# Performance work log

Measured on AMD Instinct MI355X. Metric: run time of the kernel, lower is better.

## Reference

```python
import jax, jax.numpy as jnp
import numpy as np

C = 192; G = 12; CG = C // G          # channels, groups, channels per group
KS = 3; PAD = 1; K = KS * KS - 1      # 3x3 kernel, remove_center=True -> 8 points
HID = 4 * C                           # mlp_ratio = 4
OFFSET_SCALE = 1.0

# kernel dilation grid (x, y) pairs, center removed (remove_center=True)
_pts = np.arange(KS) - (KS - 1) // 2
_gx, _gy = np.meshgrid(_pts, _pts, indexing='ij')
_grid = np.stack([_gx.ravel(), _gy.ravel()], -1).astype(np.float32)
_grid = _grid[~np.all(_grid == 0, axis=1)]   # (K, 2)
GRID = jnp.asarray(_grid)


def _ln(x, w, b, eps=1e-5):
    mu = jnp.mean(x, -1, keepdims=True)
    var = jnp.var(x, -1, keepdims=True)
    return (x - mu) * jax.lax.rsqrt(var + eps) * w + b


def _dcnv3(x, in_proj_w, in_proj_b, dw_w, dw_b, dw_ln_w, dw_ln_b,
           off_w, off_b, mask_w, mask_b, cfs_w, cfs_b, out_proj_w, out_proj_b):
    # x: (B, H, W, C) channels-last
    B, H, W, _ = x.shape
    xp = x @ in_proj_w + in_proj_b          # value / x_proj
    # depthwise conv -> LN -> GELU on the raw input (offset/mask branch)
    x1 = jax.lax.conv_general_dilated(
        x, dw_w, (1, 1), 'SAME',
        dimension_numbers=('NHWC', 'HWIO', 'NHWC'),
        feature_group_count=C) + dw_b
    x1 = jax.nn.gelu(_ln(x1, dw_ln_w, dw_ln_b, 1e-6), approximate=False)
    off = (x1 @ off_w + off_b).reshape(B, H, W, G, K, 2)      # (dx, dy) in pixels
    mask = jax.nn.softmax((x1 @ mask_w + mask_b).reshape(B, H, W, G, K), axis=-1)
    # pad value and flatten spatial; (B, Hp*Wp, G, 1, CG)
    Hp, Wp = H + 2 * PAD, W + 2 * PAD
    v = jnp.pad(xp, ((0, 0), (PAD, PAD), (PAD, PAD), (0, 0))).reshape(B, Hp * Wp, G, 1, CG)
    # sampling locations in padded-image pixel index coords (grid_sample align_corners=False)
    bx = jnp.arange(W, dtype=x.dtype)[None, None, :, None, None] + PAD
    by = jnp.arange(H, dtype=x.dtype)[None, :, None, None, None] + PAD
    px = (bx + (GRID[:, 0] + off[..., 0]) * OFFSET_SCALE).reshape(B, H * W, G, K)
    py = (by + (GRID[:, 1] + off[..., 1]) * OFFSET_SCALE).reshape(B, H * W, G, K)
    x0 = jnp.floor(px); y0 = jnp.floor(py)
    wx = px - x0; wy = py - y0
    ix0 = x0.astype(jnp.int32); iy0 = y0.astype(jnp.int32)

    def gather(iy, ix):
        valid = ((iy >= 0) & (iy < Hp) & (ix >= 0) & (ix < Wp)).astype(x.dtype)
        idx = jnp.clip(iy, 0, Hp - 1) * Wp + jnp.clip(ix, 0, Wp - 1)
        s = jnp.take_along_axis(v, idx[..., None], axis=1)    # (B, HW, G, K, CG)
        return s * valid[..., None]

    s = (gather(iy0, ix0)         * ((1 - wy) * (1 - wx))[..., None]
       + gather(iy0, ix0 + 1)     * ((1 - wy) * wx)[..., None]
       + gather(iy0 + 1, ix0)     * (wy * (1 - wx))[..., None]
       + gather(iy0 + 1, ix0 + 1) * (wy * wx)[..., None])
    out = jnp.einsum('bngk,bngkc->bngc', mask.reshape(B, H * W, G, K), s).reshape(B, H, W, C)
    # center feature scale
    cfs = jax.nn.sigmoid(x1 @ cfs_w.T + cfs_b)                # (B, H, W, G)
    cfs = jnp.repeat(cfs, CG, axis=-1)                        # (B, H, W, C)
    out = out * (1 - cfs) + xp * cfs
    return out @ out_proj_w + out_proj_b


def _forward(x, norm1_w, norm1_b, norm2_w, norm2_b, rpn1_w, rpn1_b, rpn2_w, rpn2_b,
             in_proj_w, in_proj_b, dw_w, dw_b, dw_ln_w, dw_ln_b, off_w, off_b,
             mask_w, mask_b, cfs_w, cfs_b, out_proj_w, out_proj_b,
             fc1_w, fc1_b, fc2_w, fc2_b):
    d = _dcnv3(_ln(x, norm1_w, norm1_b), in_proj_w, in_proj_b, dw_w, dw_b,
               dw_ln_w, dw_ln_b, off_w, off_b, mask_w, mask_b, cfs_w, cfs_b,
               out_proj_w, out_proj_b)
    x = x + _ln(d, rpn1_w, rpn1_b)                            # res_post_norm branch 1
    h = jax.nn.gelu(_ln(x, norm2_w, norm2_b) @ fc1_w + fc1_b, approximate=False) @ fc2_w + fc2_b
    x = x + _ln(h, rpn2_w, rpn2_b)                            # res_post_norm branch 2
    return x


def setup_inputs():
    key = jax.random.key(0)
    ks = jax.random.split(key, 12)
    r = lambda i, shape, s=0.02: jax.random.normal(ks[i], shape, jnp.float32) * s
    B, H, W = 4, 56, 56
    return dict(
        x=jax.random.normal(ks[0], (B, H, W, C), jnp.float32),
        norm1_w=jnp.ones((C,)), norm1_b=jnp.zeros((C,)),
        norm2_w=jnp.ones((C,)), norm2_b=jnp.zeros((C,)),
        rpn1_w=jnp.ones((C,)), rpn1_b=jnp.zeros((C,)),
        rpn2_w=jnp.ones((C,)), rpn2_b=jnp.zeros((C,)),
        in_proj_w=r(1, (C, C)), in_proj_b=jnp.zeros((C,)),
        dw_w=r(2, (KS, KS, 1, C), 0.1), dw_b=jnp.zeros((C,)),
        dw_ln_w=jnp.ones((C,)), dw_ln_b=jnp.zeros((C,)),
        off_w=r(3, (C, G * K * 2), 0.1), off_b=jnp.zeros((G * K * 2,)),
        mask_w=r(4, (C, G * K), 0.1), mask_b=jnp.zeros((G * K,)),
        cfs_w=r(5, (G, C), 0.1), cfs_b=jnp.zeros((G,)),
        out_proj_w=r(6, (C, C)), out_proj_b=jnp.zeros((C,)),
        fc1_w=r(7, (C, HID)), fc1_b=jnp.zeros((HID,)),
        fc2_w=r(8, (HID, C)), fc2_b=jnp.zeros((C,)),
    )


def reference(x, norm1_w, norm1_b, norm2_w, norm2_b, rpn1_w, rpn1_b, rpn2_w, rpn2_b,
              in_proj_w, in_proj_b, dw_w, dw_b, dw_ln_w, dw_ln_b, off_w, off_b,
              mask_w, mask_b, cfs_w, cfs_b, out_proj_w, out_proj_b,
              fc1_w, fc1_b, fc2_w, fc2_b):
    return _forward(x, norm1_w, norm1_b, norm2_w, norm2_b, rpn1_w, rpn1_b, rpn2_w, rpn2_b,
                    in_proj_w, in_proj_b, dw_w, dw_b, dw_ln_w, dw_ln_b, off_w, off_b,
                    mask_w, mask_b, cfs_w, cfs_b, out_proj_w, out_proj_b,
                    fc1_w, fc1_b, fc2_w, fc2_b)
```

## Files before the change

kernel.cpp:

```cpp
#include <hip/hip_runtime.h>
#include <hip/hip_bf16.h>
#include <math.h>


#define BATCH 4
#define HH 56
#define WW 56
#define CC 192
#define NPIX (BATCH * HH * WW)
#define XS_STR 200
#define H1S 776
#define OFS 193
#define MLS 97

typedef __hip_bfloat16 bf16;
typedef __attribute__((ext_vector_type(8))) short short8;
typedef __attribute__((ext_vector_type(4))) float float4v;

__device__ __forceinline__ float gelu_exact(float x) {
    return 0.5f * x * (1.f + erff(x * 0.70710678118654752f));
}
__device__ __forceinline__ bf16 f2b(float f) { return __float2bfloat16(f); }
__device__ __forceinline__ float b2fu(short s) {
    return __uint_as_float((unsigned)(unsigned short)s << 16);
}

__global__ __launch_bounds__(256) void prep_w_k(const float* __restrict__ inpw,
        const float* __restrict__ offw, const float* __restrict__ maskw,
        const float* __restrict__ cfsw, const float* __restrict__ outpw,
        const float* __restrict__ fc1w, const float* __restrict__ fc2w,
        bf16* __restrict__ wsB)
{
    const int i = blockIdx.x * 256 + threadIdx.x;
    bf16* inpP = wsB;
    bf16* omP  = wsB + 36864;
    bf16* outP = wsB + 95232;
    bf16* fc1P = wsB + 132096;
    bf16* fc2P = wsB + 279552;
    const int j   = i & 7;
    const int l   = (i >> 3) & 63;
    const int n15 = l & 15, q = l >> 4;
    const int grp = i >> 9;
    if (i < 36864) {
        const int t = grp / 6, c = grp - t * 6;
        const int n = 16 * t + n15, k = 32 * c + 8 * q + j;
        inpP[i] = f2b(inpw[(size_t)k * 192 + n]);
        outP[i] = f2b(outpw[(size_t)k * 192 + n]);
    }
    if (i < 58368) {
        const int t = grp / 6, c = grp - t * 6;
        const int n = 16 * t + n15, k = 32 * c + 8 * q + j;
        omP[i] = (n < 192) ? f2b(offw[(size_t)k * 192 + n])
               : (n < 288) ? f2b(maskw[(size_t)k * 96 + (n - 192)])
               : (n < 300) ? f2b(cfsw[(size_t)(n - 288) * 192 + k])
                           : f2b(0.f);
    }
    if (i < 147456) {
        const int t1 = grp / 6, c1 = grp - t1 * 6;
        const int n1 = 16 * t1 + n15, k1 = 32 * c1 + 8 * q + j;
        fc1P[i] = f2b(fc1w[(size_t)k1 * 768 + n1]);
        const int t2 = grp / 24, c2 = grp - t2 * 24;
        const int n2 = 16 * t2 + n15, k2 = 32 * c2 + 8 * q + j;
        fc2P[i] = f2b(fc2w[(size_t)k2 * 192 + n2]);
    }
}

__global__ __launch_bounds__(256) void ln_gemm8_k(const float* __restrict__ x,
        const float* __restrict__ n1w, const float* __restrict__ n1b,
        const bf16* __restrict__ wP, const float* __restrict__ bias,
        bf16* __restrict__ xn_out, bf16* __restrict__ xp_out)
{
    __shared__ __align__(16) bf16 xs[8 * XS_STR];
    const int tid = threadIdx.x;
    const int w   = tid >> 6;
    const int l   = tid & 63;
    const int n15 = l & 15;
    const int q   = l >> 4;
    const int p0  = blockIdx.x * 8;
    const int c0  = l * 4;

    #pragma unroll
    for (int rr = 0; rr < 2; rr++) {
        const int lr = 2 * w + rr;
        const int base = (p0 + lr) * CC;
        float4 v = (float4){0.f, 0.f, 0.f, 0.f};
        if (l < 48) v = *(const float4*)&x[base + c0];
        float s  = v.x + v.y + v.z + v.w;
        float qq = v.x*v.x + v.y*v.y + v.z*v.z + v.w*v.w;
        #pragma unroll
        for (int off = 32; off > 0; off >>= 1) {
            s  += __shfl_xor(s, off, 64);
            qq += __shfl_xor(qq, off, 64);
        }
        const float mu  = s * (1.f / CC);
        const float var = qq * (1.f / CC) - mu * mu;
        const float rs  = rsqrtf(var + 1e-5f);
        if (l < 48) {
            const float4 nw = *(const float4*)&n1w[c0];
            const float4 nb = *(const float4*)&n1b[c0];
            ushort4 u;
            bf16 h;
            h = f2b((v.x - mu) * rs * nw.x + nb.x); u.x = *(unsigned short*)&h;
            h = f2b((v.y - mu) * rs * nw.y + nb.y); u.y = *(unsigned short*)&h;
            h = f2b((v.z - mu) * rs * nw.z + nb.z); u.z = *(unsigned short*)&h;
            h = f2b((v.w - mu) * rs * nw.w + nb.w); u.w = *(unsigned short*)&h;
            *(ushort4*)&xs[lr * XS_STR + c0] = u;
            *(ushort4*)&xn_out[base + c0] = u;
        }
    }
    __syncthreads();

    short8 aF[6];
    #pragma unroll
    for (int c = 0; c < 6; c++)
        aF[c] = (n15 < 8)
              ? *(const short8*)&xs[n15 * XS_STR + c * 32 + q * 8]
              : (short8){0, 0, 0, 0, 0, 0, 0, 0};

    for (int t = w; t < 12; t += 4) {
        float4v acc = (float4v){0.f, 0.f, 0.f, 0.f};
        #pragma unroll
        for (int c = 0; c < 6; c++) {
            const short8 bF = *(const short8*)&wP[(size_t)((t * 6 + c) * 64 + l) * 8];
            acc = __builtin_amdgcn_mfma_f32_16x16x32_bf16(aF[c], bF, acc, 0, 0, 0);
        }
        if (q < 2) {
            const int n0 = 16 * t;
            const float bb = bias[n0 + n15];
            #pragma unroll
            for (int r = 0; r < 4; r++)
                xp_out[(size_t)(p0 + 4 * q + r) * 192 + n0 + n15] = f2b(acc[r] + bb);
        }
    }
}

__global__ __launch_bounds__(256) void sample_mlp_k(
        const bf16* __restrict__ xp, const bf16* __restrict__ xn,
        const float* __restrict__ dww, const float* __restrict__ dwb,
        const float* __restrict__ dwlnw, const float* __restrict__ dwlnb,
        const bf16* __restrict__ omP, const float* __restrict__ offb,
        const float* __restrict__ maskb, const float* __restrict__ cfsb,
        const bf16* __restrict__ wP, const float* __restrict__ bias,
        const float* __restrict__ x,
        const float* __restrict__ r1w, const float* __restrict__ r1b,
        const float* __restrict__ n2w, const float* __restrict__ n2b,
        const bf16* __restrict__ fc1P, const float* __restrict__ fc1b,
        const bf16* __restrict__ fc2P, const float* __restrict__ fc2b,
        const float* __restrict__ r2w, const float* __restrict__ r2b,
        float* __restrict__ out)
{
    __shared__ __align__(16) bf16 xs[16 * XS_STR];
    __shared__ __align__(16) char uni[16 * H1S * 2];
    __shared__ float ps[4][16], pq[4][16], ps2[4][16], pq2[4][16];

    float (*cv)[192]     = (float(*)[192])uni;
    float (*offs_l)[OFS] = (float(*)[OFS])uni;
    float (*mls_l)[MLS]  = (float(*)[MLS])(uni + 12352);
    float (*cfs_l)[16]   = (float(*)[16])(uni + 18560);
    bf16* h1             = (bf16*)uni;

    const int tid = threadIdx.x;
    const int w   = tid >> 6;
    const int l   = tid & 63;
    const int n15 = l & 15;
    const int q   = l >> 4;
    const int bid = (blockIdx.x & 7) * (NPIX / 128) + (blockIdx.x >> 3);
    const int p0  = bid * 16;

    if (tid < 192) {
        const int px  = tid / 12;
        const int ch0 = (tid - px * 12) * 16;
        const int pix = p0 + px;
        const int bimg = pix / (HH * WW);
        const int hw   = pix - bimg * (HH * WW);
        const int h    = hw / WW;
        const int wx   = hw - h * WW;
        const int ibase = bimg * (HH * WW * CC);

        float a[16];
        #pragma unroll
        for (int j = 0; j < 16; j += 4) {
            const float4 b4 = *(const float4*)&dwb[ch0 + j];
            a[j] = b4.x; a[j+1] = b4.y; a[j+2] = b4.z; a[j+3] = b4.w;
        }
        #pragma unroll
        for (int ky = 0; ky < 3; ky++) {
            const int yy = h + ky - 1;
            if (yy < 0 || yy >= HH) continue;
            #pragma unroll
            for (int kx = 0; kx < 3; kx++) {
                const int xx = wx + kx - 1;
                if (xx < 0 || xx >= WW) continue;
                const int o = ibase + (yy * WW + xx) * CC + ch0;
                const short8 v0 = *(const short8*)&xn[o];
                const short8 v1 = *(const short8*)&xn[o + 8];
                const int wo = (ky * 3 + kx) * CC + ch0;
                const float4 w0 = *(const float4*)&dww[wo];
                const float4 w1 = *(const float4*)&dww[wo + 4];
                const float4 w2 = *(const float4*)&dww[wo + 8];
                const float4 w3 = *(const float4*)&dww[wo + 12];
                a[0]  += b2fu(v0[0]) * w0.x; a[1]  += b2fu(v0[1]) * w0.y;
                a[2]  += b2fu(v0[2]) * w0.z; a[3]  += b2fu(v0[3]) * w0.w;
                a[4]  += b2fu(v0[4]) * w1.x; a[5]  += b2fu(v0[5]) * w1.y;
                a[6]  += b2fu(v0[6]) * w1.z; a[7]  += b2fu(v0[7]) * w1.w;
                a[8]  += b2fu(v1[0]) * w2.x; a[9]  += b2fu(v1[1]) * w2.y;
                a[10] += b2fu(v1[2]) * w2.z; a[11] += b2fu(v1[3]) * w2.w;
                a[12] += b2fu(v1[4]) * w3.x; a[13] += b2fu(v1[5]) * w3.y;
                a[14] += b2fu(v1[6]) * w3.z; a[15] += b2fu(v1[7]) * w3.w;
            }
        }
        #pragma unroll
        for (int j = 0; j < 16; j += 4)
            *(float4*)&cv[px][ch0 + j] = (float4){a[j], a[j+1], a[j+2], a[j+3]};
    }
    __syncthreads();

    #pragma unroll
    for (int pass = 0; pass < 4; pass++) {
        const int px = w + 4 * pass;
        float v[3];
        #pragma unroll
        for (int i = 0; i < 3; i++) v[i] = cv[px][l + 64 * i];
        float s = v[0] + v[1] + v[2];
        float qq = v[0]*v[0] + v[1]*v[1] + v[2]*v[2];
        #pragma unroll
        for (int off = 32; off > 0; off >>= 1) {
            s  += __shfl_xor(s, off, 64);
            qq += __shfl_xor(qq, off, 64);
        }
        const float mu  = s * (1.f / CC);
        const float var = qq * (1.f / CC) - mu * mu;
        const float rs  = rsqrtf(var + 1e-6f);
        #pragma unroll
        for (int i = 0; i < 3; i++) {
            const int c = l + 64 * i;
            xs[px * XS_STR + c] = f2b(gelu_exact((v[i] - mu) * rs * dwlnw[c] + dwlnb[c]));
        }
    }
    __syncthreads();

    {
        short8 aF[6];
        #pragma unroll
        for (int c = 0; c < 6; c++)
            aF[c] = *(const short8*)&xs[n15 * XS_STR + c * 32 + q * 8];

        for (int t = w; t < 19; t += 4) {
            float4v acc = (float4v){0.f, 0.f, 0.f, 0.f};
            #pragma unroll
            for (int c = 0; c < 6; c++) {
                const short8 bF = *(const short8*)&omP[(size_t)((t * 6 + c) * 64 + l) * 8];
                acc = __builtin_amdgcn_mfma_f32_16x16x32_bf16(aF[c], bF, acc, 0, 0, 0);
            }
            if (t < 12) {
                const int n0 = 16 * t;
                const float bb = offb[n0 + n15];
                #pragma unroll
                for (int r = 0; r < 4; r++)
                    offs_l[4 * q + r][n0 + n15] = acc[r] + bb;
            } else if (t < 18) {
                const int m0 = 16 * t - 192;
                const float bb = maskb[m0 + n15];
                #pragma unroll
                for (int r = 0; r < 4; r++) {
                    const float vv = acc[r] + bb;
                    float mx = vv;
                    mx = fmaxf(mx, __shfl_xor(mx, 1, 64));
                    mx = fmaxf(mx, __shfl_xor(mx, 2, 64));
                    mx = fmaxf(mx, __shfl_xor(mx, 4, 64));
                    const float e = __expf(vv - mx);
                    float se = e;
                    se += __shfl_xor(se, 1, 64);
                    se += __shfl_xor(se, 2, 64);
                    se += __shfl_xor(se, 4, 64);
                    mls_l[4 * q + r][m0 + n15] = e * (1.f / se);
                }
            } else {
                const float bb = (n15 < 12) ? cfsb[n15] : 0.f;
                #pragma unroll
                for (int r = 0; r < 4; r++) {
                    const float cf = 1.f / (1.f + __expf(-(acc[r] + bb)));
                    if (n15 < 12) cfs_l[4 * q + r][n15] = cf;
                }
            }
        }
    }
    __syncthreads();

    if (tid < 192) {
        const int px  = tid / 12;
        const int g   = tid - px * 12;
        const int ch0 = g * 16;
        const int pix = p0 + px;
        const int bimg = pix / (HH * WW);
        const int hw   = pix - bimg * (HH * WW);
        const int h    = hw / WW;
        const int wxp  = hw - h * WW;
        const int ibase = bimg * (HH * WW * CC);

        const float cf = cfs_l[px][g];

        float acc[16];
        #pragma unroll
        for (int j = 0; j < 16; j++) acc[j] = 0.f;

        #pragma unroll 2
        for (int k = 0; k < 8; k++) {
            const int kk = k + (k >= 4 ? 1 : 0);
            const int gx = kk / 3 - 1;
            const int gy = kk - (kk / 3) * 3 - 1;
            const float mk  = mls_l[px][g * 8 + k];
            const float px_ = (float)(wxp + gx) + offs_l[px][g * 16 + 2 * k];
            const float py_ = (float)(h   + gy) + offs_l[px][g * 16 + 2 * k + 1];
            const float fx = floorf(px_), fy = floorf(py_);
            const float wxf = px_ - fx, wyf = py_ - fy;
            const int x0 = (int)fx, y0 = (int)fy;
            const float vx0 = ((unsigned)x0       < WW) ? 1.f : 0.f;
            const float vx1 = ((unsigned)(x0 + 1) < WW) ? 1.f : 0.f;
            const float vy0 = ((unsigned)y0       < HH) ? 1.f : 0.f;
            const float vy1 = ((unsigned)(y0 + 1) < HH) ? 1.f : 0.f;
            const int x0c = min(max(x0, 0), WW - 1);
            const int x1c = min(max(x0 + 1, 0), WW - 1);
            const int y0c = min(max(y0, 0), HH - 1);
            const int y1c = min(max(y0 + 1, 0), HH - 1);
            const float wx0 = (1.f - wxf) * vx0, wx1 = wxf * vx1;
            const float wy0 = (1.f - wyf) * vy0, wy1 = wyf * vy1;
            const float w00 = mk * wy0 * wx0, w01 = mk * wy0 * wx1;
            const float w10 = mk * wy1 * wx0, w11 = mk * wy1 * wx1;
            const int r0 = ibase + y0c * (WW * CC) + ch0;
            const int r1 = ibase + y1c * (WW * CC) + ch0;
            const int o00 = r0 + x0c * CC, o01 = r0 + x1c * CC;
            const int o10 = r1 + x0c * CC, o11 = r1 + x1c * CC;
            const short8 a00 = *(const short8*)&xp[o00];
            const short8 b00 = *(const short8*)&xp[o00 + 8];
            const short8 a01 = *(const short8*)&xp[o01];
            const short8 b01 = *(const short8*)&xp[o01 + 8];
            const short8 a10 = *(const short8*)&xp[o10];
            const short8 b10 = *(const short8*)&xp[o10 + 8];
            const short8 a11 = *(const short8*)&xp[o11];
            const short8 b11 = *(const short8*)&xp[o11 + 8];
            #pragma unroll
            for (int j = 0; j < 8; j++) {
                acc[j]     += w00 * b2fu(a00[j]) + w01 * b2fu(a01[j])
                            + w10 * b2fu(a10[j]) + w11 * b2fu(a11[j]);
                acc[8 + j] += w00 * b2fu(b00[j]) + w01 * b2fu(b01[j])
                            + w10 * b2fu(b10[j]) + w11 * b2fu(b11[j]);
            }
        }

        const int po = pix * CC + ch0;
        const short8 xv0 = *(const short8*)&xp[po];
        const short8 xv1 = *(const short8*)&xp[po + 8];
        short8 o0, o1;
        #pragma unroll
        for (int j = 0; j < 8; j++) {
            const float v0 = acc[j]     * (1.f - cf) + b2fu(xv0[j]) * cf;
            const float v1 = acc[8 + j] * (1.f - cf) + b2fu(xv1[j]) * cf;
            bf16 hh;
            hh = f2b(v0); o0[j] = *(short*)&hh;
            hh = f2b(v1); o1[j] = *(short*)&hh;
        }
        *(short8*)&xs[px * XS_STR + ch0]     = o0;
        *(short8*)&xs[px * XS_STR + ch0 + 8] = o1;
    }
    __syncthreads();

    {
        short8 aF[6];
        #pragma unroll
        for (int c = 0; c < 6; c++)
            aF[c] = *(const short8*)&xs[n15 * XS_STR + c * 32 + q * 8];

        float4v acc[3];
        #pragma unroll
        for (int t = 0; t < 3; t++) {
            const int tile = 3 * w + t;
            acc[t] = (float4v){0.f, 0.f, 0.f, 0.f};
            #pragma unroll
            for (int c = 0; c < 6; c++) {
                const short8 bF = *(const short8*)&wP[(size_t)((tile * 6 + c) * 64 + l) * 8];
                acc[t] = __builtin_amdgcn_mfma_f32_16x16x32_bf16(aF[c], bF, acc[t], 0, 0, 0);
            }
            const float bb = bias[16 * tile + n15];
            #pragma unroll
            for (int r = 0; r < 4; r++) acc[t][r] += bb;
        }

        #pragma unroll
        for (int r = 0; r < 4; r++) {
            float sp = acc[0][r] + acc[1][r] + acc[2][r];
            float qp = acc[0][r]*acc[0][r] + acc[1][r]*acc[1][r] + acc[2][r]*acc[2][r];
            #pragma unroll
            for (int o = 1; o < 16; o <<= 1) {
                sp += __shfl_xor(sp, o, 64);
                qp += __shfl_xor(qp, o, 64);
            }
            if (n15 == 0) { ps[w][4 * q + r] = sp; pq[w][4 * q + r] = qp; }
        }
        __syncthreads();

        float x2v[3][4];
        #pragma unroll
        for (int r = 0; r < 4; r++) {
            const int row = 4 * q + r;
            const float s  = ps[0][row] + ps[1][row] + ps[2][row] + ps[3][row];
            const float qq = pq[0][row] + pq[1][row] + pq[2][row] + pq[3][row];
            const float mu  = s * (1.f / CC);
            const float var = qq * (1.f / CC) - mu * mu;
            const float rs  = rsqrtf(var + 1e-5f);
            const size_t grow = p0 + row;
            #pragma unroll
            for (int t = 0; t < 3; t++) {
                const int col = 48 * w + 16 * t + n15;
                x2v[t][r] = x[grow * CC + col] + (acc[t][r] - mu) * rs * r1w[col] + r1b[col];
            }
        }
        #pragma unroll
        for (int r = 0; r < 4; r++) {
            float sp = x2v[0][r] + x2v[1][r] + x2v[2][r];
            float qp = x2v[0][r]*x2v[0][r] + x2v[1][r]*x2v[1][r] + x2v[2][r]*x2v[2][r];
            #pragma unroll
            for (int o = 1; o < 16; o <<= 1) {
                sp += __shfl_xor(sp, o, 64);
                qp += __shfl_xor(qp, o, 64);
            }
            if (n15 == 0) { ps2[w][4 * q + r] = sp; pq2[w][4 * q + r] = qp; }
        }
        __syncthreads();

        #pragma unroll
        for (int r = 0; r < 4; r++) {
            const int row = 4 * q + r;
            const float s  = ps2[0][row] + ps2[1][row] + ps2[2][row] + ps2[3][row];
            const float qq = pq2[0][row] + pq2[1][row] + pq2[2][row] + pq2[3][row];
            const float mu  = s * (1.f / CC);
            const float var = qq * (1.f / CC) - mu * mu;
            const float rs  = rsqrtf(var + 1e-5f);
            #pragma unroll
            for (int t = 0; t < 3; t++) {
                const int col = 48 * w + 16 * t + n15;
                xs[row * XS_STR + col] = f2b((x2v[t][r] - mu) * rs * n2w[col] + n2b[col]);
            }
        }
        __syncthreads();

        short8 aF2[6];
        #pragma unroll
        for (int c = 0; c < 6; c++)
            aF2[c] = *(const short8*)&xs[n15 * XS_STR + c * 32 + q * 8];

        #pragma unroll
        for (int t1 = 0; t1 < 12; t1++) {
            const int tile = 12 * w + t1;
            float4v a1 = (float4v){0.f, 0.f, 0.f, 0.f};
            #pragma unroll
            for (int c = 0; c < 6; c++) {
                const short8 bF = *(const short8*)&fc1P[(size_t)((tile * 6 + c) * 64 + l) * 8];
                a1 = __builtin_amdgcn_mfma_f32_16x16x32_bf16(aF2[c], bF, a1, 0, 0, 0);
            }
            const int n0 = 16 * tile;
            const float bb = fc1b[n0 + n15];
            #pragma unroll
            for (int r = 0; r < 4; r++)
                h1[(4 * q + r) * H1S + n0 + n15] = f2b(gelu_exact(a1[r] + bb));
        }
        __syncthreads();

        float4v acc2[3];
        #pragma unroll
        for (int t = 0; t < 3; t++) acc2[t] = (float4v){0.f, 0.f, 0.f, 0.f};
        #pragma unroll 4
        for (int kc = 0; kc < 24; kc++) {
            const short8 a2 = *(const short8*)&h1[n15 * H1S + kc * 32 + q * 8];
            #pragma unroll
            for (int t = 0; t < 3; t++) {
                const int tile = 3 * w + t;
                const short8 bF = *(const short8*)&fc2P[(size_t)((tile * 24 + kc) * 64 + l) * 8];
                acc2[t] = __builtin_amdgcn_mfma_f32_16x16x32_bf16(a2, bF, acc2[t], 0, 0, 0);
            }
        }
        #pragma unroll
        for (int t = 0; t < 3; t++) {
            const float bb = fc2b[48 * w + 16 * t + n15];
            #pragma unroll
            for (int r = 0; r < 4; r++) acc2[t][r] += bb;
        }

        #pragma unroll
        for (int r = 0; r < 4; r++) {
            float sp = acc2[0][r] + acc2[1][r] + acc2[2][r];
            float qp = acc2[0][r]*acc2[0][r] + acc2[1][r]*acc2[1][r] + acc2[2][r]*acc2[2][r];
            #pragma unroll
            for (int o = 1; o < 16; o <<= 1) {
                sp += __shfl_xor(sp, o, 64);
                qp += __shfl_xor(qp, o, 64);
            }
            if (n15 == 0) { ps[w][4 * q + r] = sp; pq[w][4 * q + r] = qp; }
        }
        __syncthreads();

        #pragma unroll
        for (int r = 0; r < 4; r++) {
            const int row = 4 * q + r;
            const float s  = ps[0][row] + ps[1][row] + ps[2][row] + ps[3][row];
            const float qq = pq[0][row] + pq[1][row] + pq[2][row] + pq[3][row];
            const float mu  = s * (1.f / CC);
            const float var = qq * (1.f / CC) - mu * mu;
            const float rs  = rsqrtf(var + 1e-5f);
            const size_t grow = p0 + row;
            #pragma unroll
            for (int t = 0; t < 3; t++) {
                const int col = 48 * w + 16 * t + n15;
                out[grow * CC + col] = x2v[t][r]
                                     + (acc2[t][r] - mu) * rs * r2w[col] + r2b[col];
            }
        }
    }
}

extern "C" void kernel_launch(void* const* d_in, const int* in_sizes, int n_in,
                              void* d_out, int out_size, void* d_ws, size_t ws_size,
                              hipStream_t stream) {
    const float* x      = (const float*)d_in[0];
    const float* n1w    = (const float*)d_in[1];
    const float* n1b    = (const float*)d_in[2];
    const float* n2w    = (const float*)d_in[3];
    const float* n2b    = (const float*)d_in[4];
    const float* rpn1w  = (const float*)d_in[5];
    const float* rpn1b  = (const float*)d_in[6];
    const float* rpn2w  = (const float*)d_in[7];
    const float* rpn2b  = (const float*)d_in[8];
    const float* inpw   = (const float*)d_in[9];
    const float* inpb   = (const float*)d_in[10];
    const float* dww    = (const float*)d_in[11];
    const float* dwb    = (const float*)d_in[12];
    const float* dwlnw  = (const float*)d_in[13];
    const float* dwlnb  = (const float*)d_in[14];
    const float* offw   = (const float*)d_in[15];
    const float* offb   = (const float*)d_in[16];
    const float* maskw  = (const float*)d_in[17];
    const float* maskb  = (const float*)d_in[18];
    const float* cfsw   = (const float*)d_in[19];
    const float* cfsb   = (const float*)d_in[20];
    const float* outpw  = (const float*)d_in[21];
    const float* outpb  = (const float*)d_in[22];
    const float* fc1w   = (const float*)d_in[23];
    const float* fc1b   = (const float*)d_in[24];
    const float* fc2w   = (const float*)d_in[25];
    const float* fc2b   = (const float*)d_in[26];

    const int N = NPIX;
    const size_t NP = (size_t)N * CC;
    bf16* B0  = (bf16*)d_ws;
    bf16* B1  = B0 + NP;
    bf16* wsB = B1 + NP;
    const bf16* inpP = wsB;
    const bf16* omP  = wsB + 36864;
    const bf16* outP = wsB + 95232;
    const bf16* fc1P = wsB + 132096;
    const bf16* fc2P = wsB + 279552;

    const int g16 = N / 16;

    prep_w_k<<<576, 256, 0, stream>>>(inpw, offw, maskw, cfsw, outpw, fc1w, fc2w, wsB);
    ln_gemm8_k<<<N / 8, 256, 0, stream>>>(x, n1w, n1b, inpP, inpb, B0, B1);
    sample_mlp_k<<<g16, 256, 0, stream>>>(B1, B0, dww, dwb, dwlnw, dwlnb,
                                          omP, offb, maskb, cfsb,
                                          outP, outpb, x, rpn1w, rpn1b,
                                          n2w, n2b, fc1P, fc1b, fc2P, fc2b,
                                          rpn2w, rpn2b, (float*)d_out);
}
```

Measured before the change: 179.9 us.

## Double block size of fused sample/MLP kernel to 512 threads with 8 waves

New measurement: 210.3 us. +16.9%, slower.

```diff
diff --git a/kernel.cpp b/kernel.cpp
--- a/kernel.cpp
+++ b/kernel.cpp
@@ -134,7 +134,7 @@
     }
 }
 
-__global__ __launch_bounds__(256) void sample_mlp_k(
+__global__ __launch_bounds__(512) void sample_mlp_k(
         const bf16* __restrict__ xp, const bf16* __restrict__ xn,
         const float* __restrict__ dww, const float* __restrict__ dwb,
         const float* __restrict__ dwlnw, const float* __restrict__ dwlnb,
@@ -151,7 +151,7 @@
 {
     __shared__ __align__(16) bf16 xs[16 * XS_STR];
     __shared__ __align__(16) char uni[16 * H1S * 2];
-    __shared__ float ps[4][16], pq[4][16], ps2[4][16], pq2[4][16];
+    __shared__ float ps[8][16], pq[8][16], ps2[8][16], pq2[8][16];
 
     float (*cv)[192]     = (float(*)[192])uni;
     float (*offs_l)[OFS] = (float(*)[OFS])uni;
@@ -167,9 +167,10 @@
     const int bid = (blockIdx.x & 7) * (NPIX / 128) + (blockIdx.x >> 3);
     const int p0  = bid * 16;
 
-    if (tid < 192) {
-        const int px  = tid / 12;
-        const int ch0 = (tid - px * 12) * 16;
+    if (tid < 384) {
+        const int px  = tid / 24;
+        const int c8  = tid - px * 24;
+        const int ch0 = c8 * 8;
         const int pix = p0 + px;
         const int bimg = pix / (HH * WW);
         const int hw   = pix - bimg * (HH * WW);
@@ -177,11 +178,12 @@
         const int wx   = hw - h * WW;
         const int ibase = bimg * (HH * WW * CC);
 
-        float a[16];
-        #pragma unroll
-        for (int j = 0; j < 16; j += 4) {
-            const float4 b4 = *(const float4*)&dwb[ch0 + j];
-            a[j] = b4.x; a[j+1] = b4.y; a[j+2] = b4.z; a[j+3] = b4.w;
+        float a[8];
+        {
+            const float4 b0 = *(const float4*)&dwb[ch0];
+            const float4 b1 = *(const float4*)&dwb[ch0 + 4];
+            a[0]=b0.x; a[1]=b0.y; a[2]=b0.z; a[3]=b0.w;
+            a[4]=b1.x; a[5]=b1.y; a[6]=b1.z; a[7]=b1.w;
         }
         #pragma unroll
         for (int ky = 0; ky < 3; ky++) {
@@ -191,33 +193,24 @@
             for (int kx = 0; kx < 3; kx++) {
                 const int xx = wx + kx - 1;
                 if (xx < 0 || xx >= WW) continue;
-                const int o = ibase + (yy * WW + xx) * CC + ch0;
-                const short8 v0 = *(const short8*)&xn[o];
-                const short8 v1 = *(const short8*)&xn[o + 8];
+                const short8 v0 = *(const short8*)&xn[ibase + (yy * WW + xx) * CC + ch0];
                 const int wo = (ky * 3 + kx) * CC + ch0;
                 const float4 w0 = *(const float4*)&dww[wo];
                 const float4 w1 = *(const float4*)&dww[wo + 4];
-                const float4 w2 = *(const float4*)&dww[wo + 8];
-                const float4 w3 = *(const float4*)&dww[wo + 12];
-                a[0]  += b2fu(v0[0]) * w0.x; a[1]  += b2fu(v0[1]) * w0.y;
-                a[2]  += b2fu(v0[2]) * w0.z; a[3]  += b2fu(v0[3]) * w0.w;
-                a[4]  += b2fu(v0[4]) * w1.x; a[5]  += b2fu(v0[5]) * w1.y;
-                a[6]  += b2fu(v0[6]) * w1.z; a[7]  += b2fu(v0[7]) * w1.w;
-                a[8]  += b2fu(v1[0]) * w2.x; a[9]  += b2fu(v1[1]) * w2.y;
-                a[10] += b2fu(v1[2]) * w2.z; a[11] += b2fu(v1[3]) * w2.w;
-                a[12] += b2fu(v1[4]) * w3.x; a[13] += b2fu(v1[5]) * w3.y;
-                a[14] += b2fu(v1[6]) * w3.z; a[15] += b2fu(v1[7]) * w3.w;
-            }
-        }
-        #pragma unroll
-        for (int j = 0; j < 16; j += 4)
-            *(float4*)&cv[px][ch0 + j] = (float4){a[j], a[j+1], a[j+2], a[j+3]};
+                a[0] += b2fu(v0[0]) * w0.x; a[1] += b2fu(v0[1]) * w0.y;
+                a[2] += b2fu(v0[2]) * w0.z; a[3] += b2fu(v0[3]) * w0.w;
+                a[4] += b2fu(v0[4]) * w1.x; a[5] += b2fu(v0[5]) * w1.y;
+                a[6] += b2fu(v0[6]) * w1.z; a[7] += b2fu(v0[7]) * w1.w;
+            }
+        }
+        *(float4*)&cv[px][ch0]     = (float4){a[0], a[1], a[2], a[3]};
+        *(float4*)&cv[px][ch0 + 4] = (float4){a[4], a[5], a[6], a[7]};
     }
     __syncthreads();
 
     #pragma unroll
-    for (int pass = 0; pass < 4; pass++) {
-        const int px = w + 4 * pass;
+    for (int pass = 0; pass < 2; pass++) {
+        const int px = w + 8 * pass;
         float v[3];
         #pragma unroll
         for (int i = 0; i < 3; i++) v[i] = cv[px][l + 64 * i];
@@ -245,7 +238,7 @@
         for (int c = 0; c < 6; c++)
             aF[c] = *(const short8*)&xs[n15 * XS_STR + c * 32 + q * 8];
 
-        for (int t = w; t < 19; t += 4) {
+        for (int t = w; t < 19; t += 8) {
             float4v acc = (float4v){0.f, 0.f, 0.f, 0.f};
             #pragma unroll
             for (int c = 0; c < 6; c++) {
@@ -287,10 +280,11 @@
     }
     __syncthreads();
 
-    if (tid < 192) {
-        const int px  = tid / 12;
-        const int g   = tid - px * 12;
-        const int ch0 = g * 16;
+    if (tid < 384) {
+        const int px  = tid / 24;
+        const int s2  = tid - px * 24;
+        const int g   = s2 >> 1;
+        const int ch0 = g * 16 + (s2 & 1) * 8;
         const int pix = p0 + px;
         const int bimg = pix / (HH * WW);
         const int hw   = pix - bimg * (HH * WW);
@@ -300,9 +294,9 @@
 
         const float cf = cfs_l[px][g];
 
-        float acc[16];
-        #pragma unroll
-        for (int j = 0; j < 16; j++) acc[j] = 0.f;
+        float acc[8];
+        #pragma unroll
+        for (int j = 0; j < 8; j++) acc[j] = 0.f;
 
         #pragma unroll 2
         for (int k = 0; k < 8; k++) {
@@ -329,39 +323,26 @@
             const float w10 = mk * wy1 * wx0, w11 = mk * wy1 * wx1;
             const int r0 = ibase + y0c * (WW * CC) + ch0;
             const int r1 = ibase + y1c * (WW * CC) + ch0;
-            const int o00 = r0 + x0c * CC, o01 = r0 + x1c * CC;
-            const int o10 = r1 + x0c * CC, o11 = r1 + x1c * CC;
-            const short8 a00 = *(const short8*)&xp[o00];
-            const short8 b00 = *(const short8*)&xp[o00 + 8];
-            const short8 a01 = *(const short8*)&xp[o01];
-            const short8 b01 = *(const short8*)&xp[o01 + 8];
-            const short8 a10 = *(const short8*)&xp[o10];
-            const short8 b10 = *(const short8*)&xp[o10 + 8];
-            const short8 a11 = *(const short8*)&xp[o11];
-            const short8 b11 = *(const short8*)&xp[o11 + 8];
+            const short8 a00 = *(const short8*)&xp[r0 + x0c * CC];
+            const short8 a01 = *(const short8*)&xp[r0 + x1c * CC];
+            const short8 a10 = *(const short8*)&xp[r1 + x0c * CC];
+            const short8 a11 = *(const short8*)&xp[r1 + x1c * CC];
             #pragma unroll
             for (int j = 0; j < 8; j++) {
-                acc[j]     += w00 * b2fu(a00[j]) + w01 * b2fu(a01[j])
-                            + w10 * b2fu(a10[j]) + w11 * b2fu(a11[j]);
-                acc[8 + j] += w00 * b2fu(b00[j]) + w01 * b2fu(b01[j])
-                            + w10 * b2fu(b10[j]) + w11 * b2fu(b11[j]);
-            }
-        }
-
-        const int po = pix * CC + ch0;
-        const short8 xv0 = *(const short8*)&xp[po];
-        const short8 xv1 = *(const short8*)&xp[po + 8];
-        short8 o0, o1;
+                acc[j] += w00 * b2fu(a00[j]) + w01 * b2fu(a01[j])
+                        + w10 * b2fu(a10[j]) + w11 * b2fu(a11[j]);
+            }
+        }
+
+        const short8 xv = *(const short8*)&xp[pix * CC + ch0];
+        short8 o;
         #pragma unroll
         for (int j = 0; j < 8; j++) {
-            const float v0 = acc[j]     * (1.f - cf) + b2fu(xv0[j]) * cf;
-            const float v1 = acc[8 + j] * (1.f - cf) + b2fu(xv1[j]) * cf;
-            bf16 hh;
-            hh = f2b(v0); o0[j] = *(short*)&hh;
-            hh = f2b(v1); o1[j] = *(short*)&hh;
-        }
-        *(short8*)&xs[px * XS_STR + ch0]     = o0;
-        *(short8*)&xs[px * XS_STR + ch0 + 8] = o1;
+            const float ov = acc[j] * (1.f - cf) + b2fu(xv[j]) * cf;
+            bf16 hh = f2b(ov);
+            o[j] = *(short*)&hh;
+        }
+        *(short8*)&xs[px * XS_STR + ch0] = o;
     }
     __syncthreads();
 
@@ -371,25 +352,28 @@
         for (int c = 0; c < 6; c++)
             aF[c] = *(const short8*)&xs[n15 * XS_STR + c * 32 + q * 8];
 
-        float4v acc[3];
-        #pragma unroll
-        for (int t = 0; t < 3; t++) {
-            const int tile = 3 * w + t;
-            acc[t] = (float4v){0.f, 0.f, 0.f, 0.f};
-            #pragma unroll
-            for (int c = 0; c < 6; c++) {
-                const short8 bF = *(const short8*)&wP[(size_t)((tile * 6 + c) * 64 + l) * 8];
-                acc[t] = __builtin_amdgcn_mfma_f32_16x16x32_bf16(aF[c], bF, acc[t], 0, 0, 0);
-            }
-            const float bb = bias[16 * tile + n15];
-            #pragma unroll
-            for (int r = 0; r < 4; r++) acc[t][r] += bb;
+        float4v acc[2];
+        acc[0] = (float4v){0.f, 0.f, 0.f, 0.f};
+        acc[1] = (float4v){0.f, 0.f, 0.f, 0.f};
+        #pragma unroll
+        for (int k = 0; k < 2; k++) {
+            const int tile = w + 8 * k;
+            if (tile < 12) {
+                #pragma unroll
+                for (int c = 0; c < 6; c++) {
+                    const short8 bF = *(const short8*)&wP[(size_t)((tile * 6 + c) * 64 + l) * 8];
+                    acc[k] = __builtin_amdgcn_mfma_f32_16x16x32_bf16(aF[c], bF, acc[k], 0, 0, 0);
+                }
+                const float bb = bias[16 * tile + n15];
+                #pragma unroll
+                for (int r = 0; r < 4; r++) acc[k][r] += bb;
+            }
         }
 
         #pragma unroll
         for (int r = 0; r < 4; r++) {
-            float sp = acc[0][r] + acc[1][r] + acc[2][r];
-            float qp = acc[0][r]*acc[0][r] + acc[1][r]*acc[1][r] + acc[2][r]*acc[2][r];
+            float sp = acc[0][r] + acc[1][r];
+            float qp = acc[0][r]*acc[0][r] + acc[1][r]*acc[1][r];
             #pragma unroll
             for (int o = 1; o < 16; o <<= 1) {
                 sp += __shfl_xor(sp, o, 64);
@@ -399,26 +383,35 @@
         }
         __syncthreads();
 
-        float x2v[3][4];
+        float x2v[2][4];
+        #pragma unroll
+        for (int k = 0; k < 2; k++)
+            #pragma unroll
+            for (int r = 0; r < 4; r++) x2v[k][r] = 0.f;
+
         #pragma unroll
         for (int r = 0; r < 4; r++) {
             const int row = 4 * q + r;
-            const float s  = ps[0][row] + ps[1][row] + ps[2][row] + ps[3][row];
-            const float qq = pq[0][row] + pq[1][row] + pq[2][row] + pq[3][row];
+            float s = 0.f, qq = 0.f;
+            #pragma unroll
+            for (int ww = 0; ww < 8; ww++) { s += ps[ww][row]; qq += pq[ww][row]; }
             const float mu  = s * (1.f / CC);
             const float var = qq * (1.f / CC) - mu * mu;
             const float rs  = rsqrtf(var + 1e-5f);
             const size_t grow = p0 + row;
             #pragma unroll
-            for (int t = 0; t < 3; t++) {
-                const int col = 48 * w + 16 * t + n15;
-                x2v[t][r] = x[grow * CC + col] + (acc[t][r] - mu) * rs * r1w[col] + r1b[col];
+            for (int k = 0; k < 2; k++) {
+                const int tile = w + 8 * k;
+                if (tile < 12) {
+                    const int col = 16 * tile + n15;
+                    x2v[k][r] = x[grow * CC + col] + (acc[k][r] - mu) * rs * r1w[col] + r1b[col];
+                }
             }
         }
         #pragma unroll
         for (int r = 0; r < 4; r++) {
-            float sp = x2v[0][r] + x2v[1][r] + x2v[2][r];
-            float qp = x2v[0][r]*x2v[0][r] + x2v[1][r]*x2v[1][r] + x2v[2][r]*x2v[2][r];
+            float sp = x2v[0][r] + x2v[1][r];
+            float qp = x2v[0][r]*x2v[0][r] + x2v[1][r]*x2v[1][r];
             #pragma unroll
             for (int o = 1; o < 16; o <<= 1) {
                 sp += __shfl_xor(sp, o, 64);
@@ -431,15 +424,19 @@
         #pragma unroll
         for (int r = 0; r < 4; r++) {
             const int row = 4 * q + r;
-            const float s  = ps2[0][row] + ps2[1][row] + ps2[2][row] + ps2[3][row];
-            const float qq = pq2[0][row] + pq2[1][row] + pq2[2][row] + pq2[3][row];
+            float s = 0.f, qq = 0.f;
+            #pragma unroll
+            for (int ww = 0; ww < 8; ww++) { s += ps2[ww][row]; qq += pq2[ww][row]; }
             const float mu  = s * (1.f / CC);
             const float var = qq * (1.f / CC) - mu * mu;
             const float rs  = rsqrtf(var + 1e-5f);
             #pragma unroll
-            for (int t = 0; t < 3; t++) {
-                const int col = 48 * w + 16 * t + n15;
-                xs[row * XS_STR + col] = f2b((x2v[t][r] - mu) * rs * n2w[col] + n2b[col]);
+            for (int k = 0; k < 2; k++) {
+                const int tile = w + 8 * k;
+                if (tile < 12) {
+                    const int col = 16 * tile + n15;
+                    xs[row * XS_STR + col] = f2b((x2v[k][r] - mu) * rs * n2w[col] + n2b[col]);
+                }
             }
         }
         __syncthreads();
@@ -450,8 +447,8 @@
             aF2[c] = *(const short8*)&xs[n15 * XS_STR + c * 32 + q * 8];
 
         #pragma unroll
-        for (int t1 = 0; t1 < 12; t1++) {
-            const int tile = 12 * w + t1;
+        for (int t1 = 0; t1 < 6; t1++) {
+            const int tile = w + 8 * t1;
             float4v a1 = (float4v){0.f, 0.f, 0.f, 0.f};
             #pragma unroll
             for (int c = 0; c < 6; c++) {
@@ -466,30 +463,35 @@
         }
         __syncthreads();
 
-        float4v acc2[3];
-        #pragma unroll
-        for (int t = 0; t < 3; t++) acc2[t] = (float4v){0.f, 0.f, 0.f, 0.f};
+        float4v acc2[2];
+        acc2[0] = (float4v){0.f, 0.f, 0.f, 0.f};
+        acc2[1] = (float4v){0.f, 0.f, 0.f, 0.f};
         #pragma unroll 4
         for (int kc = 0; kc < 24; kc++) {
             const short8 a2 = *(const short8*)&h1[n15 * H1S + kc * 32 + q * 8];
             #pragma unroll
-            for (int t = 0; t < 3; t++) {
-                const int tile = 3 * w + t;
-                const short8 bF = *(const short8*)&fc2P[(size_t)((tile * 24 + kc) * 64 + l) * 8];
-                acc2[t] = __builtin_amdgcn_mfma_f32_16x16x32_bf16(a2, bF, acc2[t], 0, 0, 0);
-            }
-        }
-        #pragma unroll
-        for (int t = 0; t < 3; t++) {
-            const float bb = fc2b[48 * w + 16 * t + n15];
-            #pragma unroll
-            for (int r = 0; r < 4; r++) acc2[t][r] += bb;
+            for (int k = 0; k < 2; k++) {
+                const int tile = w + 8 * k;
+                if (tile < 12) {
+                    const short8 bF = *(const short8*)&fc2P[(size_t)((tile * 24 + kc) * 64 + l) * 8];
+                    acc2[k] = __builtin_amdgcn_mfma_f32_16x16x32_bf16(a2, bF, acc2[k], 0, 0, 0);
+                }
+            }
+        }
+        #pragma unroll
+        for (int k = 0; k < 2; k++) {
+            const int tile = w + 8 * k;
+            if (tile < 12) {
+                const float bb = fc2b[16 * tile + n15];
+                #pragma unroll
+                for (int r = 0; r < 4; r++) acc2[k][r] += bb;
+            }
         }
 
         #pragma unroll
         for (int r = 0; r < 4; r++) {
-            float sp = acc2[0][r] + acc2[1][r] + acc2[2][r];
-            float qp = acc2[0][r]*acc2[0][r] + acc2[1][r]*acc2[1][r] + acc2[2][r]*acc2[2][r];
+            float sp = acc2[0][r] + acc2[1][r];
+            float qp = acc2[0][r]*acc2[0][r] + acc2[1][r]*acc2[1][r];
             #pragma unroll
             for (int o = 1; o < 16; o <<= 1) {
                 sp += __shfl_xor(sp, o, 64);
@@ -502,17 +504,21 @@
         #pragma unroll
         for (int r = 0; r < 4; r++) {
             const int row = 4 * q + r;
-            const float s  = ps[0][row] + ps[1][row] + ps[2][row] + ps[3][row];
-            const float qq = pq[0][row] + pq[1][row] + pq[2][row] + pq[3][row];
+            float s = 0.f, qq = 0.f;
+            #pragma unroll
+            for (int ww = 0; ww < 8; ww++) { s += ps[ww][row]; qq += pq[ww][row]; }
             const float mu  = s * (1.f / CC);
             const float var = qq * (1.f / CC) - mu * mu;
             const float rs  = rsqrtf(var + 1e-5f);
             const size_t grow = p0 + row;
             #pragma unroll
-            for (int t = 0; t < 3; t++) {
-                const int col = 48 * w + 16 * t + n15;
-                out[grow * CC + col] = x2v[t][r]
-                                     + (acc2[t][r] - mu) * rs * r2w[col] + r2b[col];
+            for (int k = 0; k < 2; k++) {
+                const int tile = w + 8 * k;
+                if (tile < 12) {
+                    const int col = 16 * tile + n15;
+                    out[grow * CC + col] = x2v[k][r]
+                                         + (acc2[k][r] - mu) * rs * r2w[col] + r2b[col];
+                }
             }
         }
     }
@@ -564,7 +570,7 @@
 
     prep_w_k<<<576, 256, 0, stream>>>(inpw, offw, maskw, cfsw, outpw, fc1w, fc2w, wsB);
     ln_gemm8_k<<<N / 8, 256, 0, stream>>>(x, n1w, n1b, inpP, inpb, B0, B1);
-    sample_mlp_k<<<g16, 256, 0, stream>>>(B1, B0, dww, dwb, dwlnw, dwlnb,
+    sample_mlp_k<<<g16, 512, 0, stream>>>(B1, B0, dww, dwb, dwlnw, dwlnb,
                                           omP, offb, maskb, cfsb,
                                           outP, outpb, x, rpn1w, rpn1b,
                                           n2w, n2b, fc1P, fc1b, fc2P, fc2b,
```
